# Performance work log

Hardware: AMD Instinct MI355X
Metric: run time of the kernel (lower is better)

The kernel has to match this reference:

```python
import jax, jax.numpy as jnp
import numpy as np

NUM_HEAD = 16


def setup_inputs() -> dict:
    key = jax.random.key(0)
    k1, k2, k3 = jax.random.split(key, 3)
    E = 1024
    x = jax.random.normal(k1, (4, 2048, E), dtype=jnp.float32)
    W1 = jax.random.normal(k2, (E, 3 * E), dtype=jnp.float32) * 0.02
    b1 = jnp.zeros((3 * E,), dtype=jnp.float32)
    W2 = jax.random.normal(k3, (E, E), dtype=jnp.float32) * 0.02
    b2 = jnp.zeros((E,), dtype=jnp.float32)
    return {"x": x, "W1": W1, "b1": b1, "W2": W2, "b2": b2}


def reference(x, W1, b1, W2, b2):
    # Fused QKV projection: (n, s, 3E)
    h = x @ W1 + b1
    n, s, _ = h.shape
    # Split into heads FIRST (matches torch reshape), then transpose: (n, H, s, 3*d_head)
    h = h.reshape(n, s, NUM_HEAD, -1).transpose(0, 2, 1, 3)
    # Chunk last dim into q, k, v: each (n, H, s, d_head)
    q, k, v = jnp.split(h, 3, axis=-1)
    dk = jnp.asarray(v.shape[-1], x.dtype) ** 0.5
    # Naive full S x S attention (faithful to source)
    w = jnp.einsum("nhqd,nhkd->nhqk", q, k) / dk
    w = jax.nn.softmax(w, axis=-1)  # dropout1 is identity at eval
    att = jnp.einsum("nhqk,nhkd->nhqd", w, v)
    att = att.transpose(0, 2, 1, 3).reshape(n, s, -1)  # (n, s, E)
    return att @ W2 + b2  # dropout2 identity at eval
```

## Files before the change

kernel.cpp:

```cpp
#include <hip/hip_runtime.h>
#include <math.h>
#include <stdint.h>
#include <stddef.h>


#define SEQ    2048
#define NB     4
#define E_DIM  1024
#define N1     3072
#define M_TOK  8192
#define NHEAD  16
#define DHEAD  64

typedef __attribute__((ext_vector_type(4))) float    floatx4;
typedef __attribute__((ext_vector_type(8))) short    shortx8;
typedef __attribute__((ext_vector_type(4))) short    shortx4;
typedef __attribute__((ext_vector_type(4))) unsigned short ushortx4;

#if __has_builtin(__builtin_amdgcn_exp2f)
#define EXP2(x) __builtin_amdgcn_exp2f(x)
#else
#define EXP2(x) __expf((x) * 0.6931471805599453f)
#endif

#define MFMA_K16(a, b, c) \
    __builtin_amdgcn_mfma_f32_16x16x16bf16_1k((a), (b), (c), 0, 0, 0)

__device__ __forceinline__ unsigned short f2bf(float f) {
    union { float f; unsigned u; } v; v.f = f;
    unsigned r = (v.u + 0x7FFFu + ((v.u >> 16) & 1u)) >> 16;
    return (unsigned short)r;
}
__device__ __forceinline__ unsigned fbits(float f) {
    union { float f; unsigned u; } v; v.f = f; return v.u;
}

__device__ __forceinline__ void gl_lds16(const void* g, void* l) {
    __builtin_amdgcn_global_load_lds(
        (const __attribute__((address_space(1))) unsigned int*)g,
        (__attribute__((address_space(3))) unsigned int*)l, 16, 0, 0);
}

__global__ __launch_bounds__(256) void cvt_bf16(
    const float* __restrict__ in, unsigned short* __restrict__ out)
{
    const size_t i = ((size_t)blockIdx.x * 256 + threadIdx.x) * 8;
    float4 a = *(const float4*)(in + i);
    float4 b = *(const float4*)(in + i + 4);
    ushortx4 o0 = { f2bf(a.x), f2bf(a.y), f2bf(a.z), f2bf(a.w) };
    ushortx4 o1 = { f2bf(b.x), f2bf(b.y), f2bf(b.z), f2bf(b.w) };
    *(ushortx4*)(out + i)     = o0;
    *(ushortx4*)(out + i + 4) = o1;
}

__global__ __launch_bounds__(256) void cvt_transpose(
    const float* __restrict__ W, unsigned short* __restrict__ Wt, int K, int N)
{
    __shared__ unsigned short tile[32][33];
    const int tx = threadIdx.x, ty = threadIdx.y;
    const int n0 = blockIdx.x * 32, k0 = blockIdx.y * 32;
#pragma unroll
    for (int r = 0; r < 4; ++r) {
        const int k = ty + r * 8;
        tile[tx][k] = f2bf(W[(size_t)(k0 + k) * N + n0 + tx]);
    }
    __syncthreads();
#pragma unroll
    for (int r = 0; r < 4; ++r) {
        const int n = ty + r * 8;
        Wt[(size_t)(n0 + n) * K + k0 + tx] = tile[n][tx];
    }
}

template <bool OUT_BF16, bool FUSE>
__global__ __launch_bounds__(256) void gemm_bf16(
    const short* __restrict__ A, const short* __restrict__ Bt,
    const float* __restrict__ bias, void* __restrict__ Cout,
    unsigned short* __restrict__ Vt,
    int M, int N, int K)
{
    __shared__ short As[128 * 32];
    __shared__ short Bs[128 * 32];

    const int t    = threadIdx.x;
    const int lane = t & 63, w = t >> 6;
    const int quad = lane >> 4, l15 = lane & 15;
    const int bm = blockIdx.y * 128, bn = blockIdx.x * 128;
    const int m0w = (w >> 1) * 64, n0w = (w & 1) * 64;

    const int lrow = lane >> 2;
    const int lcol = (lane & 3) * 8;
    const short* Ag0 = A  + (size_t)(bm + (2 * w + 0) * 16 + lrow) * K + lcol;
    const short* Ag1 = A  + (size_t)(bm + (2 * w + 1) * 16 + lrow) * K + lcol;
    const short* Bg0 = Bt + (size_t)(bn + (2 * w + 0) * 16 + lrow) * K + lcol;
    const short* Bg1 = Bt + (size_t)(bn + (2 * w + 1) * 16 + lrow) * K + lcol;
    short* Al0 = As + (2 * w + 0) * 512;
    short* Al1 = As + (2 * w + 1) * 512;
    short* Bl0 = Bs + (2 * w + 0) * 512;
    short* Bl1 = Bs + (2 * w + 1) * 512;

    floatx4 acc[4][4];
#pragma unroll
    for (int i = 0; i < 4; ++i)
#pragma unroll
        for (int j = 0; j < 4; ++j) acc[i][j] = (floatx4)0.f;

    for (int k0 = 0; k0 < K; k0 += 32) {
        __syncthreads();
        gl_lds16(Ag0, Al0); gl_lds16(Ag1, Al1);
        gl_lds16(Bg0, Bl0); gl_lds16(Bg1, Bl1);
        Ag0 += 32; Ag1 += 32; Bg0 += 32; Bg1 += 32;
        __syncthreads();

        shortx8 af[4], bf[4];
#pragma unroll
        for (int mi = 0; mi < 4; ++mi)
            af[mi] = *(const shortx8*)(As + (m0w + mi * 16 + l15) * 32 + quad * 8);
#pragma unroll
        for (int ni = 0; ni < 4; ++ni)
            bf[ni] = *(const shortx8*)(Bs + (n0w + ni * 16 + l15) * 32 + quad * 8);
#pragma unroll
        for (int mi = 0; mi < 4; ++mi)
#pragma unroll
            for (int ni = 0; ni < 4; ++ni)
                acc[mi][ni] = __builtin_amdgcn_mfma_f32_16x16x32_bf16(
                    af[mi], bf[ni], acc[mi][ni], 0, 0, 0);
    }

    float bv[4];
#pragma unroll
    for (int ni = 0; ni < 4; ++ni) bv[ni] = bias[bn + n0w + ni * 16 + l15];

#pragma unroll
    for (int ni = 0; ni < 4; ++ni) {
        const int col   = bn + n0w + ni * 16 + l15;
        const int cm    = col % 192;
        const int vhead = col / 192;
#pragma unroll
        for (int mi = 0; mi < 4; ++mi) {
            const int row0 = bm + m0w + mi * 16 + quad * 4;
            float v[4];
#pragma unroll
            for (int r = 0; r < 4; ++r) v[r] = acc[mi][ni][r] + bv[ni];
            if (OUT_BF16) {
                if (FUSE && cm < DHEAD) {
#pragma unroll
                    for (int r = 0; r < 4; ++r) v[r] *= 0.18033688011112042f;
                }
                unsigned short* H = (unsigned short*)Cout;
#pragma unroll
                for (int r = 0; r < 4; ++r)
                    H[(size_t)(row0 + r) * N + col] = f2bf(v[r]);
                if (FUSE && cm >= 2 * DHEAD) {
                    const int nb = row0 >> 11;
                    const int s  = row0 & 2047;
                    const int d  = cm - 2 * DHEAD;
                    ushortx4 pk = { f2bf(v[0]), f2bf(v[1]), f2bf(v[2]), f2bf(v[3]) };
                    *(ushortx4*)(Vt + ((size_t)(nb * NHEAD + vhead) * DHEAD + d) * SEQ + s) = pk;
                }
            } else {
                float* C = (float*)Cout;
#pragma unroll
                for (int r = 0; r < 4; ++r)
                    C[(size_t)(row0 + r) * N + col] = v[r];
            }
        }
    }
}

__global__ __launch_bounds__(256, 4) void attn_mfma(
    const short* __restrict__ h, const short* __restrict__ Vt,
    unsigned short* __restrict__ att)
{
    __shared__ short Ks[2][64 * 64];
    __shared__ short Vs[2][64 * 64];

    const int t    = threadIdx.x;
    const int lane = t & 63, w = t >> 6;
    const int quad = lane >> 4, l15 = lane & 15;
    const int r7   = l15 & 7;
    const int bh = blockIdx.x, n = bh >> 4, head = bh & 15;
    const int q0 = blockIdx.y * 128 + w * 32;

    const short* hQ  = h + (size_t)n * SEQ * N1 + head * (3 * DHEAD);
    const short* hK  = hQ + DHEAD;
    const short* Vtb = Vt + (size_t)bh * DHEAD * SEQ;

    const int srow = t >> 2;
    const int sc0  = (t & 3) * 2;
    const int sk   = srow & 7;
    const short* gK = hK  + (size_t)srow * N1  + sc0 * 8;
    const short* gV = Vtb + (size_t)srow * SEQ + sc0 * 8;
    const int oL0 = srow * 64 + ((sc0    ) ^ sk) * 8;
    const int oL1 = srow * 64 + ((sc0 + 1) ^ sk) * 8;

    shortx8 qf[2][2];
#pragma unroll
    for (int qt = 0; qt < 2; ++qt)
#pragma unroll
        for (int kt = 0; kt < 2; ++kt)
            qf[qt][kt] = *(const shortx8*)(hQ + (size_t)(q0 + qt * 16 + l15) * N1
                                           + kt * 32 + quad * 8);

    floatx4 O[2][4];
    floatx4 Osum[2];
#pragma unroll
    for (int qt = 0; qt < 2; ++qt) {
        Osum[qt] = (floatx4)0.f;
#pragma unroll
        for (int dt = 0; dt < 4; ++dt) O[qt][dt] = (floatx4)0.f;
    }

    const shortx4 ones = { (short)0x3F80, (short)0x3F80, (short)0x3F80, (short)0x3F80 };

    const int NT = SEQ / 64;

    int4 ka = *(const int4*)gK, kb = *(const int4*)(gK + 8);
    int4 va = *(const int4*)gV, vb = *(const int4*)(gV + 8);
    *(int4*)(&Ks[0][oL0]) = ka; *(int4*)(&Ks[0][oL1]) = kb;
    *(int4*)(&Vs[0][oL0]) = va; *(int4*)(&Vs[0][oL1]) = vb;
    gK += (size_t)64 * N1; gV += 64;

    for (int it = 0; it < NT; ++it) {
        const int buf = it & 1;
        __syncthreads();

        const bool more = (it + 1 < NT);
        if (more) {
            ka = *(const int4*)gK; kb = *(const int4*)(gK + 8);
            va = *(const int4*)gV; vb = *(const int4*)(gV + 8);
            gK += (size_t)64 * N1; gV += 64;
        }

        const short* Kb = &Ks[buf][0];
        const short* Vb = &Vs[buf][0];

#pragma unroll
        for (int sl = 0; sl < 4; ++sl) {
            const short* krow = Kb + (sl * 16 + l15) * 64;
            shortx8 kf0 = *(const shortx8*)(krow + ((quad ^ r7) * 8));
            shortx8 kf1 = *(const shortx8*)(krow + (((quad ^ 4) ^ r7) * 8));
            shortx4 vf[4];
#pragma unroll
            for (int dt = 0; dt < 4; ++dt)
                vf[dt] = *(const shortx4*)(Vb + (dt * 16 + l15) * 64
                                           + (((sl * 4 + quad) ^ (r7 << 1)) << 2));

            shortx4 pa[2];
#pragma unroll
            for (int qt = 0; qt < 2; ++qt) {
                floatx4 s = __builtin_amdgcn_mfma_f32_16x16x32_bf16(
                    kf0, qf[qt][0], (floatx4)0.f, 0, 0, 0);
                s = __builtin_amdgcn_mfma_f32_16x16x32_bf16(
                    kf1, qf[qt][1], s, 0, 0, 0);
                const float p0 = EXP2(s[0]);
                const float p1 = EXP2(s[1]);
                const float p2 = EXP2(s[2]);
                const float p3 = EXP2(s[3]);
                union { uint2 u; shortx4 v; } cv;
                cv.u.x = __builtin_amdgcn_perm(fbits(p1), fbits(p0), 0x07060302u);
                cv.u.y = __builtin_amdgcn_perm(fbits(p3), fbits(p2), 0x07060302u);
                pa[qt] = cv.v;
            }

#pragma unroll
            for (int qt = 0; qt < 2; ++qt) {
                Osum[qt] = MFMA_K16(pa[qt], ones, Osum[qt]);
#pragma unroll
                for (int dt = 0; dt < 4; ++dt)
                    O[qt][dt] = MFMA_K16(pa[qt], vf[dt], O[qt][dt]);
            }
        }

        if (more) {
            short* Kn = &Ks[buf ^ 1][0];
            short* Vn = &Vs[buf ^ 1][0];
            *(int4*)(Kn + oL0) = ka; *(int4*)(Kn + oL1) = kb;
            *(int4*)(Vn + oL0) = va; *(int4*)(Vn + oL1) = vb;
        }
    }

    const size_t obase = ((size_t)n * SEQ + q0) * E_DIM + head * DHEAD;
#pragma unroll
    for (int qt = 0; qt < 2; ++qt)
#pragma unroll
        for (int r = 0; r < 4; ++r) {
            const float inv = 1.f / Osum[qt][r];
            const size_t row = obase + (size_t)(qt * 16 + quad * 4 + r) * E_DIM;
#pragma unroll
            for (int dt = 0; dt < 4; ++dt)
                att[row + dt * 16 + l15] = f2bf(O[qt][dt][r] * inv);
        }
}

extern "C" void kernel_launch(void* const* d_in, const int* in_sizes, int n_in,
                              void* d_out, int out_size, void* d_ws, size_t ws_size,
                              hipStream_t stream)
{
    const float* x  = (const float*)d_in[0];
    const float* W1 = (const float*)d_in[1];
    const float* b1 = (const float*)d_in[2];
    const float* W2 = (const float*)d_in[3];
    const float* b2 = (const float*)d_in[4];
    float* out = (float*)d_out;

    char* ws = (char*)d_ws;
    unsigned short* x_bf  = (unsigned short*)(ws);
    unsigned short* W1t   = (unsigned short*)(ws + (16u << 20));
    unsigned short* W2t   = (unsigned short*)(ws + (22u << 20));
    unsigned short* h_bf  = (unsigned short*)(ws + (24u << 20));
    unsigned short* attb  = (unsigned short*)(ws + (72u << 20));
    unsigned short* Vtw   = (unsigned short*)(ws + (88u << 20));

    cvt_bf16<<<dim3((M_TOK * E_DIM) / (256 * 8)), 256, 0, stream>>>(x, x_bf);
    cvt_transpose<<<dim3(N1 / 32, E_DIM / 32), dim3(32, 8), 0, stream>>>(W1, W1t, E_DIM, N1);
    cvt_transpose<<<dim3(E_DIM / 32, E_DIM / 32), dim3(32, 8), 0, stream>>>(W2, W2t, E_DIM, E_DIM);

    gemm_bf16<true, true><<<dim3(N1 / 128, M_TOK / 128), 256, 0, stream>>>(
        (const short*)x_bf, (const short*)W1t, b1, h_bf, Vtw, M_TOK, N1, E_DIM);

    attn_mfma<<<dim3(NB * NHEAD, SEQ / 128), 256, 0, stream>>>(
        (const short*)h_bf, (const short*)Vtw, attb);

    gemm_bf16<false, false><<<dim3(E_DIM / 128, M_TOK / 128), 256, 0, stream>>>(
        (const short*)attb, (const short*)W2t, b2, out, nullptr, M_TOK, E_DIM, E_DIM);
}
```

Before: 283.8 us.

## Deepen GEMM K-tile with swizzled LDS and compute softmax sums on VALU

The GEMM now loads a 64-wide K slice per iteration, using an XOR-swizzled LDS layout to avoid bank conflicts. This halves the number of barrier pairs per K sweep. In attention, the row-sum MFMA against a ones vector is replaced by scalar accumulation of the exp values plus a cross-lane shuffle reduction at the end. s_setprio is also raised around the MFMA-heavy inner loop. Together these cut matrix-core work and synchronisation, at the cost of doubled LDS use per GEMM block and extra shuffles.

```diff
diff --git a/kernel.cpp b/kernel.cpp
--- a/kernel.cpp
+++ b/kernel.cpp
@@ -79,8 +79,8 @@
     unsigned short* __restrict__ Vt,
     int M, int N, int K)
 {
-    __shared__ short As[128 * 32];
-    __shared__ short Bs[128 * 32];
+    __shared__ short As[128 * 64];
+    __shared__ short Bs[128 * 64];
 
     const int t    = threadIdx.x;
     const int lane = t & 63, w = t >> 6;
@@ -88,16 +88,13 @@
     const int bm = blockIdx.y * 128, bn = blockIdx.x * 128;
     const int m0w = (w >> 1) * 64, n0w = (w & 1) * 64;
 
-    const int lrow = lane >> 2;
-    const int lcol = (lane & 3) * 8;
-    const short* Ag0 = A  + (size_t)(bm + (2 * w + 0) * 16 + lrow) * K + lcol;
-    const short* Ag1 = A  + (size_t)(bm + (2 * w + 1) * 16 + lrow) * K + lcol;
-    const short* Bg0 = Bt + (size_t)(bn + (2 * w + 0) * 16 + lrow) * K + lcol;
-    const short* Bg1 = Bt + (size_t)(bn + (2 * w + 1) * 16 + lrow) * K + lcol;
-    short* Al0 = As + (2 * w + 0) * 512;
-    short* Al1 = As + (2 * w + 1) * 512;
-    short* Bl0 = Bs + (2 * w + 0) * 512;
-    short* Bl1 = Bs + (2 * w + 1) * 512;
+    const int srow   = t >> 3;
+    const int schunk = t & 7;
+    const int gch    = schunk ^ (srow & 7);
+    const short* Ag = A  + (size_t)(bm + srow) * K + gch * 8;
+    const short* Bg = Bt + (size_t)(bn + srow) * K + gch * 8;
+    short* Al = As + srow * 64 + schunk * 8;
+    short* Bl = Bs + srow * 64 + schunk * 8;
 
     floatx4 acc[4][4];
 #pragma unroll
@@ -105,26 +102,33 @@
 #pragma unroll
         for (int j = 0; j < 4; ++j) acc[i][j] = (floatx4)0.f;
 
-    for (int k0 = 0; k0 < K; k0 += 32) {
+    for (int k0 = 0; k0 < K; k0 += 64) {
         __syncthreads();
-        gl_lds16(Ag0, Al0); gl_lds16(Ag1, Al1);
-        gl_lds16(Bg0, Bl0); gl_lds16(Bg1, Bl1);
-        Ag0 += 32; Ag1 += 32; Bg0 += 32; Bg1 += 32;
+#pragma unroll
+        for (int r = 0; r < 4; ++r) {
+            gl_lds16(Ag + (size_t)(r * 32) * K + k0, Al + r * 32 * 64);
+            gl_lds16(Bg + (size_t)(r * 32) * K + k0, Bl + r * 32 * 64);
+        }
         __syncthreads();
 
-        shortx8 af[4], bf[4];
-#pragma unroll
-        for (int mi = 0; mi < 4; ++mi)
-            af[mi] = *(const shortx8*)(As + (m0w + mi * 16 + l15) * 32 + quad * 8);
-#pragma unroll
-        for (int ni = 0; ni < 4; ++ni)
-            bf[ni] = *(const shortx8*)(Bs + (n0w + ni * 16 + l15) * 32 + quad * 8);
-#pragma unroll
-        for (int mi = 0; mi < 4; ++mi)
+#pragma unroll
+        for (int kk = 0; kk < 2; ++kk) {
+            shortx8 af[4], bf[4];
+#pragma unroll
+            for (int mi = 0; mi < 4; ++mi)
+                af[mi] = *(const shortx8*)(As + (m0w + mi * 16 + l15) * 64
+                                           + (((kk * 4 + quad) ^ (l15 & 7)) * 8));
 #pragma unroll
             for (int ni = 0; ni < 4; ++ni)
-                acc[mi][ni] = __builtin_amdgcn_mfma_f32_16x16x32_bf16(
-                    af[mi], bf[ni], acc[mi][ni], 0, 0, 0);
+                bf[ni] = *(const shortx8*)(Bs + (n0w + ni * 16 + l15) * 64
+                                           + (((kk * 4 + quad) ^ (l15 & 7)) * 8));
+#pragma unroll
+            for (int mi = 0; mi < 4; ++mi)
+#pragma unroll
+                for (int ni = 0; ni < 4; ++ni)
+                    acc[mi][ni] = __builtin_amdgcn_mfma_f32_16x16x32_bf16(
+                        af[mi], bf[ni], acc[mi][ni], 0, 0, 0);
+        }
     }
 
     float bv[4];
@@ -203,15 +207,11 @@
                                            + kt * 32 + quad * 8);
 
     floatx4 O[2][4];
-    floatx4 Osum[2];
-#pragma unroll
-    for (int qt = 0; qt < 2; ++qt) {
-        Osum[qt] = (floatx4)0.f;
+    float lsum[2] = { 0.f, 0.f };
+#pragma unroll
+    for (int qt = 0; qt < 2; ++qt)
 #pragma unroll
         for (int dt = 0; dt < 4; ++dt) O[qt][dt] = (floatx4)0.f;
-    }
-
-    const shortx4 ones = { (short)0x3F80, (short)0x3F80, (short)0x3F80, (short)0x3F80 };
 
     const int NT = SEQ / 64;
 
@@ -235,6 +235,7 @@
         const short* Kb = &Ks[buf][0];
         const short* Vb = &Vs[buf][0];
 
+        __builtin_amdgcn_s_setprio(1);
 #pragma unroll
         for (int sl = 0; sl < 4; ++sl) {
             const short* krow = Kb + (sl * 16 + l15) * 64;
@@ -257,6 +258,7 @@
                 const float p1 = EXP2(s[1]);
                 const float p2 = EXP2(s[2]);
                 const float p3 = EXP2(s[3]);
+                lsum[qt] += (p0 + p1) + (p2 + p3);
                 union { uint2 u; shortx4 v; } cv;
                 cv.u.x = __builtin_amdgcn_perm(fbits(p1), fbits(p0), 0x07060302u);
                 cv.u.y = __builtin_amdgcn_perm(fbits(p3), fbits(p2), 0x07060302u);
@@ -264,13 +266,12 @@
             }
 
 #pragma unroll
-            for (int qt = 0; qt < 2; ++qt) {
-                Osum[qt] = MFMA_K16(pa[qt], ones, Osum[qt]);
+            for (int qt = 0; qt < 2; ++qt)
 #pragma unroll
                 for (int dt = 0; dt < 4; ++dt)
                     O[qt][dt] = MFMA_K16(pa[qt], vf[dt], O[qt][dt]);
-            }
-        }
+        }
+        __builtin_amdgcn_s_setprio(0);
 
         if (more) {
             short* Kn = &Ks[buf ^ 1][0];
@@ -280,12 +281,18 @@
         }
     }
 
+#pragma unroll
+    for (int qt = 0; qt < 2; ++qt) {
+        lsum[qt] += __shfl_xor(lsum[qt], 16);
+        lsum[qt] += __shfl_xor(lsum[qt], 32);
+    }
+
     const size_t obase = ((size_t)n * SEQ + q0) * E_DIM + head * DHEAD;
 #pragma unroll
     for (int qt = 0; qt < 2; ++qt)
 #pragma unroll
         for (int r = 0; r < 4; ++r) {
-            const float inv = 1.f / Osum[qt][r];
+            const float inv = 1.f / __shfl(lsum[qt], quad * 4 + r);
             const size_t row = obase + (size_t)(qt * 16 + quad * 4 + r) * E_DIM;
 #pragma unroll
             for (int dt = 0; dt < 4; ++dt)
```

Result: faster. 277.9 us (-2.0%).
